# Kernel optimization log

Measured on AMD Instinct MI355X. Metric: run time of the kernel, lower is better.

## Reference

```python
import jax, jax.numpy as jnp
import numpy as np
from functools import partial

H = 64  # hidden_size
F = 5   # num_features
ALPHA_RANK = 1.0
NEG_SLOPE = 0.2


def setup_inputs() -> dict:
    key = jax.random.key(0)
    ks = jax.random.split(key, 10)
    N, T = 4096, 512
    feature = jax.random.normal(ks[0], (N, T, F), dtype=jnp.float32)
    ret = jax.random.normal(ks[1], (N,), dtype=jnp.float32)
    mask = jax.random.bernoulli(ks[2], 0.9, (N,))
    s = 1.0 / np.sqrt(H)
    Wih = jax.random.uniform(ks[3], (4 * H, F), jnp.float32, -s, s)
    Whh = jax.random.uniform(ks[4], (4 * H, H), jnp.float32, -s, s)
    bih = jax.random.uniform(ks[5], (4 * H,), jnp.float32, -s, s)
    bhh = jax.random.uniform(ks[6], (4 * H,), jnp.float32, -s, s)
    Wd = jax.random.uniform(ks[7], (1, H), jnp.float32, -s, s)
    bd = jax.random.uniform(ks[8], (1,), jnp.float32, -s, s)
    return {"feature": feature, "ret": ret, "mask": mask,
            "Wih": Wih, "Whh": Whh, "bih": bih, "bhh": bhh,
            "Wd": Wd, "bd": bd}


def _lstm_last_h(x, Wih, Whh, bih, bhh):
    # x: [N, T, F] -> last hidden state [N, H]. PyTorch gate order: i, f, g, o.
    N = x.shape[0]
    b = bih + bhh
    # precompute input projections for all steps: [T, N, 4H]
    x_proj = jnp.einsum('ntf,gf->tng', x, Wih) + b

    def step(carry, xt):
        h, c = carry
        gates = xt + h @ Whh.T  # [N, 4H]
        i, f, g, o = jnp.split(gates, 4, axis=-1)
        i = jax.nn.sigmoid(i)
        f = jax.nn.sigmoid(f)
        g = jnp.tanh(g)
        o = jax.nn.sigmoid(o)
        c = f * c + i * g
        h = o * jnp.tanh(c)
        return (h, c), None

    h0 = jnp.zeros((N, H), x.dtype)
    c0 = jnp.zeros((N, H), x.dtype)
    (h, _), _ = jax.lax.scan(step, (h0, c0), x_proj)
    return h


def _masked_mse(pred, gt, mask):
    m = mask.astype(pred.dtype)
    return jnp.sum((pred - gt) ** 2 * m) / (jnp.sum(m) + 1e-8)


def _rank_loss(pred, gt, mask):
    m = mask.astype(pred.dtype)
    pred_diff = pred[None, :] - pred[:, None]   # [i,j] = pred[j]-pred[i]
    true_diff = gt[None, :] - gt[:, None]
    mm = m[None, :] * m[:, None]
    return jnp.mean(jax.nn.relu(-pred_diff * true_diff * mm))


def reference(feature, ret, mask, Wih, Whh, bih, bhh, Wd, bd):
    h_last = _lstm_last_h(feature, Wih, Whh, bih, bhh)          # [N, H]
    pred = jax.nn.leaky_relu(h_last @ Wd.T + bd, NEG_SLOPE)[:, 0]  # [N]
    reg_loss = _masked_mse(pred, ret, mask)
    rank_loss = _rank_loss(pred, ret, mask)
    loss = reg_loss + ALPHA_RANK * rank_loss
    return pred, loss, reg_loss, rank_loss
```

## Files before the change

### kernel.cpp

```cpp
#include <hip/hip_runtime.h>

#define NSEQ   4096
#define TSTEPS 512
#define FIN    5
#define HID    64
#define SPB    16
#define BLK    512

typedef __attribute__((ext_vector_type(8))) short bsh8;
typedef __attribute__((ext_vector_type(4))) float f32x4;
typedef __attribute__((ext_vector_type(2))) float f32x2;
typedef __attribute__((ext_vector_type(4))) int   i32x4;

#define MFMA16(A, B, C) __builtin_amdgcn_mfma_f32_16x16x32_bf16((A), (B), (C), 0, 0, 0)

#define LOG2E 1.4426950408889634f
#define SNEG  (-LOG2E)
#define SPOS  (2.0f * LOG2E)

struct Frag2 { bsh8 hi; bsh8 lo; };

__device__ __forceinline__ unsigned short bf16hi_rn(float x) {
    unsigned u = __float_as_uint(x);
    return (unsigned short)((u + 0x7fffu + ((u >> 16) & 1u)) >> 16);
}
__device__ __forceinline__ void split_bf16(float v, unsigned short& h, unsigned short& l) {
    h = bf16hi_rn(v);
    float hf_ = __uint_as_float(((unsigned)h) << 16);
    l = bf16hi_rn(v - hf_);
}

__device__ __forceinline__ Frag2 load_whh_frag(const float* __restrict__ Whh, int row, int k, float scale) {
    const float* p = Whh + row * HID + k;
    Frag2 r;
#pragma unroll
    for (int j = 0; j < 8; ++j) {
        unsigned short h, l;
        split_bf16(scale * p[j], h, l);
        r.hi[j] = (short)h; r.lo[j] = (short)l;
    }
    return r;
}
__device__ __forceinline__ Frag2 load_wih_frag(const float* __restrict__ Wih,
                                               const float* __restrict__ bih,
                                               const float* __restrict__ bhh,
                                               int row, int quad, float scale) {
    Frag2 r;
#pragma unroll
    for (int j = 0; j < 8; ++j) { r.hi[j] = 0; r.lo[j] = 0; }
    if (quad == 0) {
        unsigned short h, l;
#pragma unroll
        for (int j = 0; j < FIN; ++j) {
            split_bf16(scale * Wih[row * FIN + j], h, l);
            r.hi[j] = (short)h; r.lo[j] = (short)l;
        }
        split_bf16(scale * (bih[row] + bhh[row]), h, l);
        r.hi[FIN] = (short)h; r.lo[FIN] = (short)l;
    }
    return r;
}

__device__ __forceinline__ void stage_chunk(const float* __restrict__ feat,
                                            bsh8 (*dst)[SPB],
                                            int seq0, int t0, int tid) {
#pragma unroll
    for (int it = 0; it < (64 * SPB) / BLK; ++it) {
        int idx = tid + it * BLK;
        int t2  = idx >> 4;
        int s   = idx & 15;
        const float* xp = feat + (size_t)(seq0 + s) * (TSTEPS * FIN) + (t0 + t2) * FIN;
        bsh8 v = {0, 0, 0, 0, 0, 0, 0, 0};
#pragma unroll
        for (int j = 0; j < FIN; ++j) v[j] = (short)bf16hi_rn(xp[j]);
        v[FIN] = (short)0x3F80;
        dst[t2][s] = v;
    }
}

__device__ __forceinline__ void epi2(float zi0, float zf0, float zg0, float zo0,
                                     float zi1, float zf1, float zg1, float zo1,
                                     float& cs0, float& cs1, float& h0, float& h1) {
    float Ei0 = __builtin_amdgcn_exp2f(zi0), Ei1 = __builtin_amdgcn_exp2f(zi1);
    float Ef0 = __builtin_amdgcn_exp2f(zf0), Ef1 = __builtin_amdgcn_exp2f(zf1);
    float Eg0 = __builtin_amdgcn_exp2f(zg0), Eg1 = __builtin_amdgcn_exp2f(zg1);
    float P10 = (1.0f + Ei0) * (1.0f + Eg0), Pf0 = 1.0f + Ef0;
    float P11 = (1.0f + Ei1) * (1.0f + Eg1), Pf1 = 1.0f + Ef1;
    float D0 = P10 * Pf0, D1 = P11 * Pf1;
    float Rp = __builtin_amdgcn_rcpf(D0 * D1);
    float n10 = __builtin_fmaf(SPOS, Eg0, -SPOS);
    float n11 = __builtin_fmaf(SPOS, Eg1, -SPOS);
    float m0 = __builtin_fmaf(P10, cs0, n10 * Pf0);
    float m1 = __builtin_fmaf(P11, cs1, n11 * Pf1);
    cs0 = (Rp * D1) * m0;
    cs1 = (Rp * D0) * m1;
    float Eo0 = __builtin_amdgcn_exp2f(zo0), Eo1 = __builtin_amdgcn_exp2f(zo1);
    float Ec0 = __builtin_amdgcn_exp2f(cs0), Ec1 = __builtin_amdgcn_exp2f(cs1);
    float D20 = (1.0f + Eo0) * (1.0f + Ec0);
    float D21 = (1.0f + Eo1) * (1.0f + Ec1);
    float R2p = __builtin_amdgcn_rcpf(D20 * D21);
    h0 = (Ec0 - 1.0f) * (R2p * D21);
    h1 = (Ec1 - 1.0f) * (R2p * D20);
}

__global__ __launch_bounds__(BLK)
void lstm_kernel(const float* __restrict__ feat,
                 const float* __restrict__ Wih,
                 const float* __restrict__ Whh,
                 const float* __restrict__ bih,
                 const float* __restrict__ bhh,
                 const float* __restrict__ Wd,
                 const float* __restrict__ bd,
                 float* __restrict__ pred,
                 float* __restrict__ accums) {
    __shared__ bsh8  aA[2][SPB][9];
    __shared__ bsh8  xb[2][64][SPB];
    __shared__ float hf[SPB][HID + 1];
    __shared__ float pf[SPB][17];

    const int tid   = threadIdx.x;
    const int w     = tid >> 6;
    const int lane  = tid & 63;
    const int col   = lane & 15;
    const int quad  = lane >> 4;
    const int quad4 = quad * 4;
    const int wg    = w & 3;
    const int half  = w >> 2;
    const int u     = 16 * wg + col;
    const int r0    = quad4 + 2 * half;
    const int seq0  = blockIdx.x * SPB;

    if (blockIdx.x == 0 && tid < 4) accums[tid] = 0.0f;

    {
        bsh8 z = {0, 0, 0, 0, 0, 0, 0, 0};
        if (tid < SPB * 9) (&aA[0][0][0])[tid] = z;
    }
    stage_chunk(feat, xb[0], seq0, 0, tid);

    const Frag2 b00 = load_whh_frag(Whh, 0*HID + u,      quad*8, SNEG);
    const Frag2 b01 = load_whh_frag(Whh, 0*HID + u, 32 + quad*8, SNEG);
    const Frag2 b10 = load_whh_frag(Whh, 1*HID + u,      quad*8, SNEG);
    const Frag2 b11 = load_whh_frag(Whh, 1*HID + u, 32 + quad*8, SNEG);
    const Frag2 b20 = load_whh_frag(Whh, 2*HID + u,      quad*8, SPOS);
    const Frag2 b21 = load_whh_frag(Whh, 2*HID + u, 32 + quad*8, SPOS);
    const Frag2 b30 = load_whh_frag(Whh, 3*HID + u,      quad*8, SNEG);
    const Frag2 b31 = load_whh_frag(Whh, 3*HID + u, 32 + quad*8, SNEG);
    const Frag2 w0_ = load_wih_frag(Wih, bih, bhh, 0*HID + u, quad, SNEG);
    const Frag2 w1_ = load_wih_frag(Wih, bih, bhh, 1*HID + u, quad, SNEG);
    const Frag2 w2_ = load_wih_frag(Wih, bih, bhh, 2*HID + u, quad, SPOS);
    const Frag2 w3_ = load_wih_frag(Wih, bih, bhh, 3*HID + u, quad, SNEG);

    __syncthreads();

    float cs0 = 0.f, cs1 = 0.f;
    f32x2 ps0, ps1, ps2, ps3;

    {
        bsh8 ax = xb[0][0][col];
        f32x4 e0 = {0.f,0.f,0.f,0.f}, e1 = e0, e2 = e0, e3 = e0;
        e0 = MFMA16(ax, w0_.hi, e0); e0 = MFMA16(ax, w0_.lo, e0);
        e1 = MFMA16(ax, w1_.hi, e1); e1 = MFMA16(ax, w1_.lo, e1);
        e2 = MFMA16(ax, w2_.hi, e2); e2 = MFMA16(ax, w2_.lo, e2);
        e3 = MFMA16(ax, w3_.hi, e3); e3 = MFMA16(ax, w3_.lo, e3);
        ps0 = half ? (f32x2){e0[2], e0[3]} : (f32x2){e0[0], e0[1]};
        ps1 = half ? (f32x2){e1[2], e1[3]} : (f32x2){e1[0], e1[1]};
        ps2 = half ? (f32x2){e2[2], e2[3]} : (f32x2){e2[0], e2[1]};
        ps3 = half ? (f32x2){e3[2], e3[3]} : (f32x2){e3[0], e3[1]};
    }

    unsigned short* const aAb = (unsigned short*)&aA[0][0][0];
    const int rowbase = r0 * 72 + u;
    const int aAhalf  = SPB * 9 * 8;

    for (int t = 0; t < TSTEPS; ++t) {
        const int buf = t & 1;
        const int nb  = buf ^ 1;
        __syncthreads();

        bsh8 ah0 = aA[buf][col][quad];
        bsh8 ah1 = aA[buf][col][4 + quad];

        const f32x4 zz = {0.f, 0.f, 0.f, 0.f};
        f32x4 acc0 = MFMA16(ah0, b00.hi, zz);
        f32x4 acc1 = MFMA16(ah0, b10.hi, zz);
        f32x4 acc2 = MFMA16(ah0, b20.hi, zz);
        f32x4 acc3 = MFMA16(ah0, b30.hi, zz);
        acc0 = MFMA16(ah1, b01.hi, acc0);
        acc1 = MFMA16(ah1, b11.hi, acc1);
        acc2 = MFMA16(ah1, b21.hi, acc2);
        acc3 = MFMA16(ah1, b31.hi, acc3);
        acc0 = MFMA16(ah0, b00.lo, acc0);
        acc1 = MFMA16(ah0, b10.lo, acc1);
        acc2 = MFMA16(ah0, b20.lo, acc2);
        acc3 = MFMA16(ah0, b30.lo, acc3);
        acc0 = MFMA16(ah1, b01.lo, acc0);
        acc1 = MFMA16(ah1, b11.lo, acc1);
        acc2 = MFMA16(ah1, b21.lo, acc2);
        acc3 = MFMA16(ah1, b31.lo, acc3);

        float a00 = half ? acc0[2] : acc0[0], a01 = half ? acc0[3] : acc0[1];
        float a10 = half ? acc1[2] : acc1[0], a11 = half ? acc1[3] : acc1[1];
        float a20 = half ? acc2[2] : acc2[0], a21 = half ? acc2[3] : acc2[1];
        float a30 = half ? acc3[2] : acc3[0], a31 = half ? acc3[3] : acc3[1];

        float h0, h1;
        epi2(a00 + ps0.x, a10 + ps1.x, a20 + ps2.x, a30 + ps3.x,
             a01 + ps0.y, a11 + ps1.y, a21 + ps2.y, a31 + ps3.y,
             cs0, cs1, h0, h1);

        unsigned pk;
        asm("v_cvt_pk_bf16_f32 %0, %1, %2" : "=v"(pk) : "v"(h0), "v"(h1));
        unsigned short* hp = aAb + nb * aAhalf + rowbase;
        hp[0]  = (unsigned short)pk;
        hp[72] = (unsigned short)(pk >> 16);
        if (t == TSTEPS - 1) {
            hf[r0 + 0][u] = h0;
            hf[r0 + 1][u] = h1;
        }

        if ((t & 63) == 0 && t + 64 < TSTEPS)
            stage_chunk(feat, xb[((t >> 6) + 1) & 1], seq0, ((t >> 6) + 1) * 64, tid);
        if (t + 1 < TSTEPS) {
            const int t1 = t + 1;
            bsh8 ax = xb[(t1 >> 6) & 1][t1 & 63][col];
            f32x4 e0 = {0.f,0.f,0.f,0.f}, e1 = e0, e2 = e0, e3 = e0;
            e0 = MFMA16(ax, w0_.hi, e0); e0 = MFMA16(ax, w0_.lo, e0);
            e1 = MFMA16(ax, w1_.hi, e1); e1 = MFMA16(ax, w1_.lo, e1);
            e2 = MFMA16(ax, w2_.hi, e2); e2 = MFMA16(ax, w2_.lo, e2);
            e3 = MFMA16(ax, w3_.hi, e3); e3 = MFMA16(ax, w3_.lo, e3);
            ps0 = half ? (f32x2){e0[2], e0[3]} : (f32x2){e0[0], e0[1]};
            ps1 = half ? (f32x2){e1[2], e1[3]} : (f32x2){e1[0], e1[1]};
            ps2 = half ? (f32x2){e2[2], e2[3]} : (f32x2){e2[0], e2[1]};
            ps3 = half ? (f32x2){e3[2], e3[3]} : (f32x2){e3[0], e3[1]};
        }
    }
    __syncthreads();

    if (tid < 256) {
        int s  = tid & 15;
        int hq = tid >> 4;
        int j0 = hq * 4;
        float part = hf[s][j0] * Wd[j0] + hf[s][j0 + 1] * Wd[j0 + 1]
                   + hf[s][j0 + 2] * Wd[j0 + 2] + hf[s][j0 + 3] * Wd[j0 + 3];
        pf[s][hq] = part;
    }
    __syncthreads();
    if (tid < SPB) {
        float sum = bd[0];
#pragma unroll
        for (int j = 0; j < 16; ++j) sum += pf[tid][j];
        float p = (sum >= 0.0f) ? sum : 0.2f * sum;
        pred[seq0 + tid] = p;
    }
}

__global__ __launch_bounds__(256)
void loss_kernel(const float* __restrict__ pred,
                 const float* __restrict__ ret,
                 const int* __restrict__ mask,
                 float* __restrict__ accums) {
    __shared__ __align__(16) float sp[NSEQ];
    __shared__ __align__(16) float sg_[NSEQ];
    __shared__ __align__(16) float sq[NSEQ];
    __shared__ float wsum[8];
    int tid = threadIdx.x;
    for (int idx = tid; idx < NSEQ / 4; idx += 256) {
        f32x4 p4 = ((const f32x4*)pred)[idx];
        f32x4 g4 = ((const f32x4*)ret)[idx];
        i32x4 m4 = ((const i32x4*)mask)[idx];
        f32x4 q4;
#pragma unroll
        for (int l = 0; l < 4; ++l) q4[l] = m4[l] ? 1.0f : 0.0f;
        *(f32x4*)&sp[idx * 4] = p4;
        *(f32x4*)&sg_[idx * 4] = g4;
        *(f32x4*)&sq[idx * 4] = q4;
    }
    __syncthreads();

    if (blockIdx.x == 0) {
        float v = 0.0f, m = 0.0f;
        for (int j = tid; j < NSEQ; j += 256) {
            float mj = sq[j];
            float d  = sp[j] - sg_[j];
            v += d * d * mj;
            m += mj;
        }
#pragma unroll
        for (int off = 32; off > 0; off >>= 1) {
            v += __shfl_down(v, off, 64);
            m += __shfl_down(m, off, 64);
        }
        if ((tid & 63) == 0) {
            atomicAdd(&accums[0], v);
            atomicAdd(&accums[1], m);
        }
    }

    int iloc = tid >> 5;
    int jp   = tid & 31;
    int i    = blockIdx.x * 8 + iloc;
    float pi = sp[i], gi = sg_[i], qi = sq[i];
    float sum = 0.0f;
    for (int j0 = jp * 4; j0 < NSEQ; j0 += 128) {
        f32x4 p4 = *(const f32x4*)&sp[j0];
        f32x4 g4 = *(const f32x4*)&sg_[j0];
        f32x4 q4 = *(const f32x4*)&sq[j0];
#pragma unroll
        for (int l = 0; l < 4; ++l) {
            float t = -(p4[l] - pi) * (g4[l] - gi);
            sum += fmaxf(t, 0.0f) * q4[l];
        }
    }
    sum *= qi;
#pragma unroll
    for (int off = 16; off > 0; off >>= 1) sum += __shfl_down(sum, off, 32);
    if (jp == 0) wsum[iloc] = sum;
    __syncthreads();
    if (tid == 0) {
        float s = wsum[0] + wsum[1] + wsum[2] + wsum[3]
                + wsum[4] + wsum[5] + wsum[6] + wsum[7];
        atomicAdd(&accums[2], s);
    }
}

__global__ void final_kernel(const float* __restrict__ accums,
                             float* __restrict__ out) {
    float reg  = accums[0] / (accums[1] + 1e-8f);
    float rank = accums[2] / 16777216.0f;
    out[NSEQ + 0] = reg + rank;
    out[NSEQ + 1] = reg;
    out[NSEQ + 2] = rank;
}

extern "C" void kernel_launch(void* const* d_in, const int* in_sizes, int n_in,
                              void* d_out, int out_size, void* d_ws, size_t ws_size,
                              hipStream_t stream) {
    const float* feat = (const float*)d_in[0];
    const float* ret  = (const float*)d_in[1];
    const int*   mask = (const int*)d_in[2];
    const float* Wih  = (const float*)d_in[3];
    const float* Whh  = (const float*)d_in[4];
    const float* bih  = (const float*)d_in[5];
    const float* bhh  = (const float*)d_in[6];
    const float* Wd   = (const float*)d_in[7];
    const float* bd   = (const float*)d_in[8];
    float* out    = (float*)d_out;
    float* accums = (float*)d_ws;

    lstm_kernel<<<NSEQ / SPB, BLK, 0, stream>>>(feat, Wih, Whh, bih, bhh,
                                                Wd, bd, out, accums);
    loss_kernel<<<NSEQ / 8, 256, 0, stream>>>(out, ret, mask, accums);
    final_kernel<<<1, 1, 0, stream>>>(accums, out);
}
```

Baseline: 432.7 us.

## Halve block to 4 waves and ping-pong two sequence groups across MFMA and epilogue

The block shrinks from 8 waves to 4, so each wave now owns all 16 sequences for its 16 hidden units. The 16 sequences are split into two groups, A and B, and their timesteps are interleaved: one group's recurrent MFMAs are issued while the other group's gate epilogue runs. Lane shuffles route accumulator rows to the owning lanes, and there are two barriers per step instead of one. The aim is to hide MFMA latency behind the transcendental epilogue and use fewer waves per block. In exchange, each wave issues twice as many MFMAs per step, carries more register state, and synchronises twice as often.

```diff
diff --git a/kernel.cpp b/kernel.cpp
--- a/kernel.cpp
+++ b/kernel.cpp
@@ -5,11 +5,10 @@
 #define FIN    5
 #define HID    64
 #define SPB    16
-#define BLK    512
+#define BLK    256
 
 typedef __attribute__((ext_vector_type(8))) short bsh8;
 typedef __attribute__((ext_vector_type(4))) float f32x4;
-typedef __attribute__((ext_vector_type(2))) float f32x2;
 typedef __attribute__((ext_vector_type(4))) int   i32x4;
 
 #define MFMA16(A, B, C) __builtin_amdgcn_mfma_f32_16x16x32_bf16((A), (B), (C), 0, 0, 0)
@@ -123,18 +122,14 @@
     const int lane  = tid & 63;
     const int col   = lane & 15;
     const int quad  = lane >> 4;
-    const int quad4 = quad * 4;
-    const int wg    = w & 3;
-    const int half  = w >> 2;
-    const int u     = 16 * wg + col;
-    const int r0    = quad4 + 2 * half;
+    const int u     = 16 * w + col;
     const int seq0  = blockIdx.x * SPB;
 
     if (blockIdx.x == 0 && tid < 4) accums[tid] = 0.0f;
 
     {
         bsh8 z = {0, 0, 0, 0, 0, 0, 0, 0};
-        if (tid < SPB * 9) (&aA[0][0][0])[tid] = z;
+        if (tid < SPB * 9) (&aA[1][0][0])[tid] = z;
     }
     stage_chunk(feat, xb[0], seq0, 0, tid);
 
@@ -153,91 +148,134 @@
 
     __syncthreads();
 
-    float cs0 = 0.f, cs1 = 0.f;
-    f32x2 ps0, ps1, ps2, ps3;
-
+    f32x4 sd0, sd1, sd2, sd3;
     {
-        bsh8 ax = xb[0][0][col];
-        f32x4 e0 = {0.f,0.f,0.f,0.f}, e1 = e0, e2 = e0, e3 = e0;
-        e0 = MFMA16(ax, w0_.hi, e0); e0 = MFMA16(ax, w0_.lo, e0);
-        e1 = MFMA16(ax, w1_.hi, e1); e1 = MFMA16(ax, w1_.lo, e1);
-        e2 = MFMA16(ax, w2_.hi, e2); e2 = MFMA16(ax, w2_.lo, e2);
-        e3 = MFMA16(ax, w3_.hi, e3); e3 = MFMA16(ax, w3_.lo, e3);
-        ps0 = half ? (f32x2){e0[2], e0[3]} : (f32x2){e0[0], e0[1]};
-        ps1 = half ? (f32x2){e1[2], e1[3]} : (f32x2){e1[0], e1[1]};
-        ps2 = half ? (f32x2){e2[2], e2[3]} : (f32x2){e2[0], e2[1]};
-        ps3 = half ? (f32x2){e3[2], e3[3]} : (f32x2){e3[0], e3[1]};
-    }
-
+        const f32x4 zz = {0.f, 0.f, 0.f, 0.f};
+        bsh8 ax0 = xb[0][0][col];
+        f32x4 e0 = MFMA16(ax0, w0_.hi, zz); e0 = MFMA16(ax0, w0_.lo, e0);
+        f32x4 e1 = MFMA16(ax0, w1_.hi, zz); e1 = MFMA16(ax0, w1_.lo, e1);
+        f32x4 e2 = MFMA16(ax0, w2_.hi, zz); e2 = MFMA16(ax0, w2_.lo, e2);
+        f32x4 e3 = MFMA16(ax0, w3_.hi, zz); e3 = MFMA16(ax0, w3_.lo, e3);
+        sd0 = e0; sd1 = e1; sd2 = e2; sd3 = e3;
+    }
+
+    f32x4 accA0 = {0.f,0.f,0.f,0.f}, accA1 = accA0, accA2 = accA0, accA3 = accA0;
+    float csA0 = 0.f, csA1 = 0.f, csB0 = 0.f, csB1 = 0.f;
+
+    const int rA = (quad & 1) * 4 + ((quad >> 1) ? 2 : 0);
+    const int rB = 8 + (quad & 1) * 4 + ((quad >> 1) ? 0 : 2);
     unsigned short* const aAb = (unsigned short*)&aA[0][0][0];
-    const int rowbase = r0 * 72 + u;
-    const int aAhalf  = SPB * 9 * 8;
+    const int aAhalf = SPB * 9 * 8;
 
     for (int t = 0; t < TSTEPS; ++t) {
-        const int buf = t & 1;
-        const int nb  = buf ^ 1;
-        __syncthreads();
-
-        bsh8 ah0 = aA[buf][col][quad];
-        bsh8 ah1 = aA[buf][col][4 + quad];
-
-        const f32x4 zz = {0.f, 0.f, 0.f, 0.f};
-        f32x4 acc0 = MFMA16(ah0, b00.hi, zz);
-        f32x4 acc1 = MFMA16(ah0, b10.hi, zz);
-        f32x4 acc2 = MFMA16(ah0, b20.hi, zz);
-        f32x4 acc3 = MFMA16(ah0, b30.hi, zz);
-        acc0 = MFMA16(ah1, b01.hi, acc0);
-        acc1 = MFMA16(ah1, b11.hi, acc1);
-        acc2 = MFMA16(ah1, b21.hi, acc2);
-        acc3 = MFMA16(ah1, b31.hi, acc3);
-        acc0 = MFMA16(ah0, b00.lo, acc0);
-        acc1 = MFMA16(ah0, b10.lo, acc1);
-        acc2 = MFMA16(ah0, b20.lo, acc2);
-        acc3 = MFMA16(ah0, b30.lo, acc3);
-        acc0 = MFMA16(ah1, b01.lo, acc0);
-        acc1 = MFMA16(ah1, b11.lo, acc1);
-        acc2 = MFMA16(ah1, b21.lo, acc2);
-        acc3 = MFMA16(ah1, b31.lo, acc3);
-
-        float a00 = half ? acc0[2] : acc0[0], a01 = half ? acc0[3] : acc0[1];
-        float a10 = half ? acc1[2] : acc1[0], a11 = half ? acc1[3] : acc1[1];
-        float a20 = half ? acc2[2] : acc2[0], a21 = half ? acc2[3] : acc2[1];
-        float a30 = half ? acc3[2] : acc3[0], a31 = half ? acc3[3] : acc3[1];
-
-        float h0, h1;
-        epi2(a00 + ps0.x, a10 + ps1.x, a20 + ps2.x, a30 + ps3.x,
-             a01 + ps0.y, a11 + ps1.y, a21 + ps2.y, a31 + ps3.y,
-             cs0, cs1, h0, h1);
-
-        unsigned pk;
-        asm("v_cvt_pk_bf16_f32 %0, %1, %2" : "=v"(pk) : "v"(h0), "v"(h1));
-        unsigned short* hp = aAb + nb * aAhalf + rowbase;
-        hp[0]  = (unsigned short)pk;
-        hp[72] = (unsigned short)(pk >> 16);
-        if (t == TSTEPS - 1) {
-            hf[r0 + 0][u] = h0;
-            hf[r0 + 1][u] = h1;
-        }
+        const int  qA   = t & 1;
+        const bool have = (t + 1 < TSTEPS);
+        const f32x4 zz  = {0.f, 0.f, 0.f, 0.f};
+
+        bsh8 fB0 = aA[qA ^ 1][col][quad];
+        bsh8 fB1 = aA[qA ^ 1][col][4 + quad];
+        bsh8 ax  = xb[((t + 1) >> 6) & 1][(t + 1) & 63][col];
+
+        f32x4 sA0 = accA0 + sd0, sA1 = accA1 + sd1, sA2 = accA2 + sd2, sA3 = accA3 + sd3;
+        float xi0 = __shfl_xor(sA0[2], 32, 64), xi1 = __shfl_xor(sA0[3], 32, 64);
+        float xf0 = __shfl_xor(sA1[2], 32, 64), xf1 = __shfl_xor(sA1[3], 32, 64);
+        float xg0 = __shfl_xor(sA2[2], 32, 64), xg1 = __shfl_xor(sA2[3], 32, 64);
+        float xo0 = __shfl_xor(sA3[2], 32, 64), xo1 = __shfl_xor(sA3[3], 32, 64);
+        const bool loq = (quad < 2);
+        float zi0 = loq ? sA0[0] : xi0, zi1 = loq ? sA0[1] : xi1;
+        float zf0 = loq ? sA1[0] : xf0, zf1 = loq ? sA1[1] : xf1;
+        float zg0 = loq ? sA2[0] : xg0, zg1 = loq ? sA2[1] : xg1;
+        float zo0 = loq ? sA3[0] : xo0, zo1 = loq ? sA3[1] : xo1;
+
+        f32x4 accB0 = MFMA16(fB0, b00.hi, zz);
+        f32x4 accB1 = MFMA16(fB0, b10.hi, zz);
+        f32x4 accB2 = MFMA16(fB0, b20.hi, zz);
+        f32x4 accB3 = MFMA16(fB0, b30.hi, zz);
+        accB0 = MFMA16(fB1, b01.hi, accB0);
+        accB1 = MFMA16(fB1, b11.hi, accB1);
+        accB2 = MFMA16(fB1, b21.hi, accB2);
+        accB3 = MFMA16(fB1, b31.hi, accB3);
+        accB0 = MFMA16(fB0, b00.lo, accB0);
+        accB1 = MFMA16(fB0, b10.lo, accB1);
+        accB2 = MFMA16(fB0, b20.lo, accB2);
+        accB3 = MFMA16(fB0, b30.lo, accB3);
+        accB0 = MFMA16(fB1, b01.lo, accB0);
+        accB1 = MFMA16(fB1, b11.lo, accB1);
+        accB2 = MFMA16(fB1, b21.lo, accB2);
+        accB3 = MFMA16(fB1, b31.lo, accB3);
+
+        float hA0, hA1;
+        epi2(zi0, zf0, zg0, zo0, zi1, zf1, zg1, zo1, csA0, csA1, hA0, hA1);
+        {
+            unsigned pk;
+            asm("v_cvt_pk_bf16_f32 %0, %1, %2" : "=v"(pk) : "v"(hA0), "v"(hA1));
+            unsigned short* hp = aAb + qA * aAhalf + rA * 72 + u;
+            hp[0]  = (unsigned short)pk;
+            hp[72] = (unsigned short)(pk >> 16);
+        }
+        if (t == TSTEPS - 1) { hf[rA][u] = hA0; hf[rA + 1][u] = hA1; }
 
         if ((t & 63) == 0 && t + 64 < TSTEPS)
             stage_chunk(feat, xb[((t >> 6) + 1) & 1], seq0, ((t >> 6) + 1) * 64, tid);
-        if (t + 1 < TSTEPS) {
-            const int t1 = t + 1;
-            bsh8 ax = xb[(t1 >> 6) & 1][t1 & 63][col];
-            f32x4 e0 = {0.f,0.f,0.f,0.f}, e1 = e0, e2 = e0, e3 = e0;
-            e0 = MFMA16(ax, w0_.hi, e0); e0 = MFMA16(ax, w0_.lo, e0);
-            e1 = MFMA16(ax, w1_.hi, e1); e1 = MFMA16(ax, w1_.lo, e1);
-            e2 = MFMA16(ax, w2_.hi, e2); e2 = MFMA16(ax, w2_.lo, e2);
-            e3 = MFMA16(ax, w3_.hi, e3); e3 = MFMA16(ax, w3_.lo, e3);
-            ps0 = half ? (f32x2){e0[2], e0[3]} : (f32x2){e0[0], e0[1]};
-            ps1 = half ? (f32x2){e1[2], e1[3]} : (f32x2){e1[0], e1[1]};
-            ps2 = half ? (f32x2){e2[2], e2[3]} : (f32x2){e2[0], e2[1]};
-            ps3 = half ? (f32x2){e3[2], e3[3]} : (f32x2){e3[0], e3[1]};
-        }
-    }
-    __syncthreads();
-
-    if (tid < 256) {
+
+        __syncthreads();
+
+        bsh8 fA0 = aA[qA][col][quad];
+        bsh8 fA1 = aA[qA][col][4 + quad];
+
+        f32x4 sB0 = accB0 + sd0, sB1 = accB1 + sd1, sB2 = accB2 + sd2, sB3 = accB3 + sd3;
+        float yi0 = __shfl_xor(sB0[2], 32, 64), yi1 = __shfl_xor(sB0[3], 32, 64);
+        float yf0 = __shfl_xor(sB1[2], 32, 64), yf1 = __shfl_xor(sB1[3], 32, 64);
+        float yg0 = __shfl_xor(sB2[2], 32, 64), yg1 = __shfl_xor(sB2[3], 32, 64);
+        float yo0 = __shfl_xor(sB3[2], 32, 64), yo1 = __shfl_xor(sB3[3], 32, 64);
+        const bool hiq = (quad >= 2);
+        float wi0 = hiq ? sB0[0] : yi0, wi1 = hiq ? sB0[1] : yi1;
+        float wf0 = hiq ? sB1[0] : yf0, wf1 = hiq ? sB1[1] : yf1;
+        float wg0 = hiq ? sB2[0] : yg0, wg1 = hiq ? sB2[1] : yg1;
+        float wo0 = hiq ? sB3[0] : yo0, wo1 = hiq ? sB3[1] : yo1;
+
+        if (have) {
+            f32x4 e0 = MFMA16(ax, w0_.hi, zz); e0 = MFMA16(ax, w0_.lo, e0);
+            f32x4 e1 = MFMA16(ax, w1_.hi, zz); e1 = MFMA16(ax, w1_.lo, e1);
+            f32x4 e2 = MFMA16(ax, w2_.hi, zz); e2 = MFMA16(ax, w2_.lo, e2);
+            f32x4 e3 = MFMA16(ax, w3_.hi, zz); e3 = MFMA16(ax, w3_.lo, e3);
+            sd0 = e0; sd1 = e1; sd2 = e2; sd3 = e3;
+        }
+
+        if (have) {
+            accA0 = MFMA16(fA0, b00.hi, zz);
+            accA1 = MFMA16(fA0, b10.hi, zz);
+            accA2 = MFMA16(fA0, b20.hi, zz);
+            accA3 = MFMA16(fA0, b30.hi, zz);
+            accA0 = MFMA16(fA1, b01.hi, accA0);
+            accA1 = MFMA16(fA1, b11.hi, accA1);
+            accA2 = MFMA16(fA1, b21.hi, accA2);
+            accA3 = MFMA16(fA1, b31.hi, accA3);
+            accA0 = MFMA16(fA0, b00.lo, accA0);
+            accA1 = MFMA16(fA0, b10.lo, accA1);
+            accA2 = MFMA16(fA0, b20.lo, accA2);
+            accA3 = MFMA16(fA0, b30.lo, accA3);
+            accA0 = MFMA16(fA1, b01.lo, accA0);
+            accA1 = MFMA16(fA1, b11.lo, accA1);
+            accA2 = MFMA16(fA1, b21.lo, accA2);
+            accA3 = MFMA16(fA1, b31.lo, accA3);
+        }
+
+        float hB0, hB1;
+        epi2(wi0, wf0, wg0, wo0, wi1, wf1, wg1, wo1, csB0, csB1, hB0, hB1);
+        {
+            unsigned pk;
+            asm("v_cvt_pk_bf16_f32 %0, %1, %2" : "=v"(pk) : "v"(hB0), "v"(hB1));
+            unsigned short* hp = aAb + qA * aAhalf + rB * 72 + u;
+            hp[0]  = (unsigned short)pk;
+            hp[72] = (unsigned short)(pk >> 16);
+        }
+        if (t == TSTEPS - 1) { hf[rB][u] = hB0; hf[rB + 1][u] = hB1; }
+
+        __syncthreads();
+    }
+
+    {
         int s  = tid & 15;
         int hq = tid >> 4;
         int j0 = hq * 4;
```

New measurement: 578.4 us. +33.7%, slower.
